# Optimization experiments

Hardware: AMD Instinct MI355X
Metric: run time of the kernel (lower is better)

Reference implementation:

```python
import jax, jax.numpy as jnp
import numpy as np

K_TOP = 2          # hardcoded k in MyAttentionFunction
S = 32             # hardcoded spatial size (interpolate to 32x32)
N = S * S          # 1024 patches (patch_size=1, stride=1 unfold)
NEG = jnp.float32(-1e30)  # stand-in for excluding columns from top-k


def setup_inputs() -> dict:
    key = jax.random.key(0)
    k1, k2, k3 = jax.random.split(key, 3)
    C = 4096
    generated = jax.random.normal(k1, (1, C, S, S), dtype=jnp.float32)
    known = jax.random.normal(k2, (1, C, S, S), dtype=jnp.float32)
    mask = jax.random.randint(k3, (1, 1, S, S), 0, 2).astype(jnp.float32)
    return {"generated": generated, "known": known, "mask": mask}


def _forward(generated, known, mask):
    C = generated.shape[1]
    # F.interpolate(mask, (32,32)) nearest, then flatten -> flag in {0,1}, shape (N,)
    flag = jax.image.resize(mask, (1, 1, S, S), method="nearest").reshape(N)
    # MyUnfold(x, 1, 1) == [1, N, C]; drop batch dim of 1.
    P = generated.reshape(C, N).T   # (N, C) patches of `generated`
    Kp = known.reshape(C, N).T      # (N, C) patches of `known`

    norm_p = jnp.sum(P * P, axis=-1)   # (N,)
    norm_k = jnp.sum(Kp * Kp, axis=-1)
    # Full cosine matrices; original restricts rows to flag==1 and columns to
    # flag==0 (cosine0) / flag==1 (cosine1) by extraction; we mask columns with
    # a very negative value so top-k returns the same values with GLOBAL indices
    # (which is exactly what the original reconstructs via nonzero()[indexes]).
    cos0 = (P @ Kp.T) / jnp.sqrt(norm_p[:, None] * norm_k[None, :])  # (N, N)
    cos1 = (P @ P.T) / jnp.sqrt(norm_p[:, None] * norm_p[None, :])
    cos0 = jnp.where(flag[None, :] == 0, cos0, NEG)
    cos1 = jnp.where(flag[None, :] == 1, cos1, NEG)

    w0, i0 = jax.lax.top_k(cos0, K_TOP)  # (N, k) values / global indices
    w1, i1 = jax.lax.top_k(cos1, K_TOP)

    m = flag                      # 1.0 on masked rows
    nm = jnp.sum(m)               # number of masked patches
    # weight means taken only over masked rows, then softmax (original uses
    # .item() + numpy softmax, i.e. detached constants).
    means = jnp.stack(
        [jnp.sum(w0[:, i] * m) / nm for i in range(K_TOP)]
        + [jnp.sum(w1[:, i] * m) / nm for i in range(K_TOP)]
    )
    weights = jax.lax.stop_gradient(jax.nn.softmax(means))  # (2k,)

    # The original builds dense 1024x1024 indicator matrices and bmm's them;
    # each indicator row for a masked patch is one-hot at its retrieved source,
    # so the bmm is just a gather into masked rows. The advanced-indexing quirk
    # ind[mask_idx, src_idx] (nonzero() pairs include a leading 0 column) also
    # unconditionally sets ind[0,0]=1; we reproduce that (set semantics: no
    # double count if row 0 already maps to column 0).
    rtn = jnp.zeros((N, C), dtype=generated.dtype)
    for i in range(2 * K_TOP):
        src = Kp if i < K_TOP else P
        cols = (i0 if i < K_TOP else i1)[:, i % K_TOP]  # (N,) global indices
        out_i = jnp.where(m[:, None] == 1, src[cols], 0.0)  # masked rows only
        dup = 1.0 - ((m[0] == 1) & (cols[0] == 0)).astype(src.dtype)
        out_i = out_i.at[0].add(src[0] * dup)  # spurious ind[0,0]=1 artifact
        rtn = rtn + weights[i] * out_i

    rtn = rtn.reshape(1, S, S, C).transpose(0, 3, 1, 2)  # (1, C, 32, 32)
    return jnp.concatenate([generated, known, rtn], axis=1)


def reference(generated, known, mask):
    return _forward(generated, known, mask)
```

## Files before the change

### kernel.cpp

```cpp
#include <hip/hip_runtime.h>
#include <hip/hip_bf16.h>
#include <math.h>

#define N_TOT 1024
#define C_DIM 4096
#define T_MARGIN 3e-4f

typedef __attribute__((ext_vector_type(8))) _Float16 half8;
typedef __attribute__((ext_vector_type(8))) unsigned short ushort8;
typedef __attribute__((ext_vector_type(8))) char schar8;
typedef __attribute__((ext_vector_type(4))) float floatx4;

__device__ inline unsigned short f2h(float v) {
    _Float16 h = (_Float16)v;
    return __builtin_bit_cast(unsigned short, h);
}
__device__ inline float h2f(unsigned short u) {
    return (float)__builtin_bit_cast(_Float16, u);
}
__device__ inline char lo_enc(float v, unsigned short h) {
    int e = (h >> 10) & 31;
    float lo = v - h2f(h);
    float q = rintf(lo * 240.0f * __uint_as_float((unsigned)(152 - e) << 23));
    q = fmaxf(-127.0f, fminf(127.0f, q));
    return (char)(int)q;
}
__device__ inline float lo_dec(char q, unsigned short h) {
    int e = (h >> 10) & 31;
    return (float)q * __uint_as_float((unsigned)(e + 102) << 23) * (1.0f / 240.0f);
}

__device__ inline void ins2(float v, int s, float& v1, int& s1, float& v2, int& s2) {
    if (v > v1 || (v == v1 && s < s1)) { v2 = v1; s2 = s1; v1 = v; s1 = s; }
    else if (v > v2 || (v == v2 && s < s2)) { v2 = v; s2 = s; }
}

__global__ __launch_bounds__(256) void split_norms(const float* __restrict__ G,
                                                   const float* __restrict__ Kn,
                                                   const float* __restrict__ flag,
                                                   unsigned short* __restrict__ Phi,
                                                   char* __restrict__ Plo,
                                                   unsigned short* __restrict__ Khi,
                                                   char* __restrict__ Klo,
                                                   float* __restrict__ normP,
                                                   float* __restrict__ normK,
                                                   int* __restrict__ colidx,
                                                   int* __restrict__ n0p) {
    const int z = blockIdx.z;
    const float* X = z ? Kn : G;
    unsigned short* Xhi = z ? Khi : Phi;
    char* Xlo = z ? Klo : Plo;
    float* normX = z ? normK : normP;

    __shared__ float tile[64 * 65];
    const int t  = threadIdx.x;
    const int c0 = blockIdx.x * 64;
    const int n0 = blockIdx.y * 64;

    #pragma unroll
    for (int s = 0; s < 4; s++) {
        int c_loc = s * 16 + (t >> 4);
        int n4    = (t & 15) * 4;
        float4 v = *(const float4*)&X[(size_t)(c0 + c_loc) * N_TOT + n0 + n4];
        tile[c_loc * 65 + n4 + 0] = v.x;
        tile[c_loc * 65 + n4 + 1] = v.y;
        tile[c_loc * 65 + n4 + 2] = v.z;
        tile[c_loc * 65 + n4 + 3] = v.w;
    }
    __syncthreads();

    #pragma unroll
    for (int s = 0; s < 2; s++) {
        int n_loc = s * 32 + (t >> 3);
        int c8    = (t & 7) * 8;
        unsigned short h[8]; char l[8];
        float s2 = 0.0f;
        #pragma unroll
        for (int e = 0; e < 8; e++) {
            float v = tile[(c8 + e) * 65 + n_loc];
            s2 = fmaf(v, v, s2);
            h[e] = f2h(v);
            l[e] = lo_enc(v, h[e]);
        }
        s2 += __shfl_xor(s2, 1);
        s2 += __shfl_xor(s2, 2);
        s2 += __shfl_xor(s2, 4);
        if ((t & 7) == 0) atomicAdd(&normX[n0 + n_loc], s2);

        size_t base = (size_t)(n0 + n_loc) * C_DIM + c0 + c8;
        ushort8 hv; schar8 lv;
        #pragma unroll
        for (int e = 0; e < 8; e++) { hv[e] = h[e]; lv[e] = l[e]; }
        *(ushort8*)&Xhi[base] = hv;
        *(schar8*)&Xlo[base]  = lv;
    }

    if (blockIdx.x == 0 && blockIdx.y == 0 && blockIdx.z == 0) {
        __shared__ int cz[256];
        __shared__ int co[256];
        float4 fv = *(const float4*)&flag[4 * t];
        int f[4] = {fv.x == 0.0f, fv.y == 0.0f, fv.z == 0.0f, fv.w == 0.0f};
        int nz = f[0] + f[1] + f[2] + f[3];
        cz[t] = nz; co[t] = 4 - nz;
        __syncthreads();
        for (int off = 1; off < 256; off <<= 1) {
            int vz = (t >= off) ? cz[t - off] : 0;
            int vo = (t >= off) ? co[t - off] : 0;
            __syncthreads();
            cz[t] += vz; co[t] += vo;
            __syncthreads();
        }
        const int fn0 = cz[255];
        int zs = cz[t] - nz;
        int os = fn0 + co[t] - (4 - nz);
        #pragma unroll
        for (int e = 0; e < 4; e++) {
            int j = 4 * t + e;
            if (f[e]) colidx[zs++] = j;
            else      colidx[os++] = j;
        }
        if (t == 0) *n0p = fn0;
    }
}

__global__ __launch_bounds__(256, 2) void gemm_coarse(const unsigned short* __restrict__ Phi,
                                                      const unsigned short* __restrict__ Khi,
                                                      const int* __restrict__ colidx,
                                                      const int* __restrict__ n0p,
                                                      float* __restrict__ dotPart) {
    const int n0 = *n0p;
    const int n1 = N_TOT - n0;
    const int ib = blockIdx.x * 128;
    if (ib >= n1) return;

    __shared__ unsigned short sA[128 * 64];
    __shared__ unsigned short sB[128 * 64];

    const int t    = threadIdx.x;
    const int wave = t >> 6, lane = t & 63;
    const int wm   = wave >> 1, wn = wave & 1;
    const int quad = lane >> 4, lrow = lane & 15;
    const int jb = blockIdx.y * 128;
    const int bz = blockIdx.z;
    const int k_beg = bz * 512;

    const int srow = t >> 3;
    const int g    = (t & 7) ^ (srow & 7);

    const unsigned short* gA[4];
    #pragma unroll
    for (int q = 0; q < 4; q++) {
        int r = ib + q * 32 + srow;
        int rr = (r < n1) ? r : (n1 - 1);
        int rowA = colidx[n0 + rr];
        gA[q] = Phi + (size_t)rowA * C_DIM + g * 8;
    }
    const unsigned short* gB[4];
    #pragma unroll
    for (int q = 0; q < 4; q++) {
        int s = jb + q * 32 + srow;
        int row = colidx[s];
        const unsigned short* src = (s < n0) ? Khi : Phi;
        gB[q] = src + (size_t)row * C_DIM + g * 8;
    }

    floatx4 acc[4][4] = {};

    for (int k0 = k_beg; k0 < k_beg + 512; k0 += 64) {
        #pragma unroll
        for (int q = 0; q < 4; q++)
            __builtin_amdgcn_global_load_lds(
                (const __attribute__((address_space(1))) void*)(gA[q] + k0),
                (__attribute__((address_space(3))) void*)((char*)sA + q * 4096 + t * 16), 16, 0, 0);
        #pragma unroll
        for (int q = 0; q < 4; q++)
            __builtin_amdgcn_global_load_lds(
                (const __attribute__((address_space(1))) void*)(gB[q] + k0),
                (__attribute__((address_space(3))) void*)((char*)sB + q * 4096 + t * 16), 16, 0, 0);
        __syncthreads();

        #pragma unroll
        for (int kk = 0; kk < 2; kk++) {
            const int gk = kk * 4 + quad;
            half8 a[4], b[4];
            #pragma unroll
            for (int ti = 0; ti < 4; ti++) {
                int m = wm * 64 + ti * 16 + lrow;
                a[ti] = *(const half8*)&sA[m * 64 + ((gk ^ (m & 7)) << 3)];
            }
            #pragma unroll
            for (int tj = 0; tj < 4; tj++) {
                int n = wn * 64 + tj * 16 + lrow;
                b[tj] = *(const half8*)&sB[n * 64 + ((gk ^ (n & 7)) << 3)];
            }
            #pragma unroll
            for (int ti = 0; ti < 4; ti++)
                #pragma unroll
                for (int tj = 0; tj < 4; tj++)
                    acc[ti][tj] = __builtin_amdgcn_mfma_f32_16x16x32_f16(a[ti], b[tj], acc[ti][tj], 0, 0, 0);
        }
        __syncthreads();
    }

    float* outp = dotPart + ((size_t)bz << 20);
    #pragma unroll
    for (int tj = 0; tj < 4; tj++) {
        int j = jb + wn * 64 + tj * 16 + lrow;
        #pragma unroll
        for (int ti = 0; ti < 4; ti++) {
            #pragma unroll
            for (int reg = 0; reg < 4; reg++) {
                int i = ib + wm * 64 + ti * 16 + quad * 4 + reg;
                outp[i * N_TOT + j] = acc[ti][tj][reg];
            }
        }
    }
}

__global__ __launch_bounds__(256) void select_k(const float* __restrict__ dotPart,
                                                const float* __restrict__ normP,
                                                const float* __restrict__ normK,
                                                const int* __restrict__ colidx,
                                                const int* __restrict__ n0p,
                                                float* __restrict__ w01,
                                                int* __restrict__ i01,
                                                int* __restrict__ wl_hdr,
                                                int* __restrict__ wl_cand) {
    __shared__ float sr_v1[2][4], sr_v2[2][4];
    __shared__ int   sr_s1[2][4], sr_s2[2][4];
    __shared__ int   s_cnt[2];
    __shared__ int   s_cand[2][16];

    const int r = blockIdx.x;
    const int t = threadIdx.x;
    const int n0 = *n0p;
    const int n1 = N_TOT - n0;
    if (r >= n1) {
        if (t < 2) wl_hdr[2 * r + t] = 0;
        return;
    }
    const int row = colidx[n0 + r];
    const int wave = t >> 6, lane = t & 63;
    const float nr = normP[row];

    if (t < 2) s_cnt[t] = 0;

    const float* base = dotPart + (size_t)r * N_TOT + 4 * t;
    float4 p0 = *(const float4*)(base);
    float4 p1 = *(const float4*)(base + (1ull << 20));
    float4 p2 = *(const float4*)(base + (2ull << 20));
    float4 p3 = *(const float4*)(base + (3ull << 20));
    float4 p4 = *(const float4*)(base + (4ull << 20));
    float4 p5 = *(const float4*)(base + (5ull << 20));
    float4 p6 = *(const float4*)(base + (6ull << 20));
    float4 p7 = *(const float4*)(base + (7ull << 20));
    float4 dv;
    dv.x = ((p0.x + p1.x) + (p2.x + p3.x)) + ((p4.x + p5.x) + (p6.x + p7.x));
    dv.y = ((p0.y + p1.y) + (p2.y + p3.y)) + ((p4.y + p5.y) + (p6.y + p7.y));
    dv.z = ((p0.z + p1.z) + (p2.z + p3.z)) + ((p4.z + p5.z) + (p6.z + p7.z));
    dv.w = ((p0.w + p1.w) + (p2.w + p3.w)) + ((p4.w + p5.w) + (p6.w + p7.w));

    float cv[4];
    #pragma unroll
    for (int e = 0; e < 4; e++) {
        int s = 4 * t + e;
        int gj = colidx[s];
        float nb = (s < n0) ? normK[gj] : normP[gj];
        float d  = (e == 0) ? dv.x : (e == 1) ? dv.y : (e == 2) ? dv.z : dv.w;
        cv[e] = d * rsqrtf(nr * nb);
    }

    #pragma unroll
    for (int zz = 0; zz < 2; zz++) {
        float v1 = -INFINITY, v2 = -INFINITY;
        int   s1 = 0x7FFFFFFF, s2 = 0x7FFFFFFF;
        #pragma unroll
        for (int e = 0; e < 4; e++) {
            int s = 4 * t + e;
            bool inz = zz ? (s >= n0) : (s < n0);
            if (inz) ins2(cv[e], s, v1, s1, v2, s2);
        }
        #pragma unroll
        for (int off = 32; off > 0; off >>= 1) {
            float o1 = __shfl_xor(v1, off); int q1 = __shfl_xor(s1, off);
            float o2 = __shfl_xor(v2, off); int q2 = __shfl_xor(s2, off);
            ins2(o1, q1, v1, s1, v2, s2);
            ins2(o2, q2, v1, s1, v2, s2);
        }
        if (lane == 0) {
            sr_v1[zz][wave] = v1; sr_s1[zz][wave] = s1;
            sr_v2[zz][wave] = v2; sr_s2[zz][wave] = s2;
        }
    }
    __syncthreads();

    float m1z[2], m2z[2]; int b1z[2], b2z[2];
    #pragma unroll
    for (int zz = 0; zz < 2; zz++) {
        float m1 = -INFINITY, m2 = -INFINITY;
        int   b1 = 0x7FFFFFFF, b2 = 0x7FFFFFFF;
        #pragma unroll
        for (int w = 0; w < 4; w++) {
            ins2(sr_v1[zz][w], sr_s1[zz][w], m1, b1, m2, b2);
            ins2(sr_v2[zz][w], sr_s2[zz][w], m1, b1, m2, b2);
        }
        m1z[zz] = m1; m2z[zz] = m2; b1z[zz] = b1; b2z[zz] = b2;
        const float thr = m2 - T_MARGIN;
        #pragma unroll
        for (int e = 0; e < 4; e++) {
            int s = 4 * t + e;
            bool inz = zz ? (s >= n0) : (s < n0);
            if (inz && cv[e] > thr) {
                int idx = atomicAdd(&s_cnt[zz], 1);
                if (idx < 16) s_cand[zz][idx] = s;
            }
        }
    }
    __syncthreads();

    bool need[2]; int cntz[2];
    #pragma unroll
    for (int zz = 0; zz < 2; zz++) {
        const int cnt = min(s_cnt[zz], 16);
        cntz[zz] = cnt;
        const bool trusted = (s_cnt[zz] == 2) && (m1z[zz] - m2z[zz] > T_MARGIN);
        need[zz] = !trusted;
        if (t == 0) {
            wl_hdr[2 * r + zz] = trusted ? 0 : cnt;
            if (trusted) {
                int base2 = (zz * N_TOT + row) * 2;
                w01[base2]     = m1z[zz];
                w01[base2 + 1] = m2z[zz];
                i01[base2]     = colidx[b1z[zz]];
                i01[base2 + 1] = colidx[b2z[zz]];
            }
        }
    }
    __syncthreads();

    #pragma unroll
    for (int zz = 0; zz < 2; zz++)
        if (need[zz] && t < cntz[zz])
            wl_cand[(2 * r + zz) * 16 + t] = s_cand[zz][t];
}

__global__ __launch_bounds__(256) void refine2(const unsigned short* __restrict__ Phi,
                                               const char* __restrict__ Plo,
                                               const unsigned short* __restrict__ Khi,
                                               const char* __restrict__ Klo,
                                               const float* __restrict__ normP,
                                               const float* __restrict__ normK,
                                               const int* __restrict__ colidx,
                                               const int* __restrict__ n0p,
                                               const int* __restrict__ wl_hdr,
                                               const int* __restrict__ wl_cand,
                                               float* __restrict__ w01,
                                               int* __restrict__ i01) {
    __shared__ float sAf[C_DIM];
    __shared__ float s_rcv[16];
    __shared__ int   s_rcj[16];

    const int item = blockIdx.x;
    const int cnt  = wl_hdr[item];
    if (cnt == 0) return;

    const int n0 = *n0p;
    const int r  = item >> 1;
    const int zz = item & 1;
    const int row = colidx[n0 + r];
    const int t   = threadIdx.x;
    const int grp = t >> 5, l32 = t & 31;
    const float nr = normP[row];

    {
        const unsigned short* Ah = Phi + (size_t)row * C_DIM;
        const char*           Al = Plo + (size_t)row * C_DIM;
        #pragma unroll
        for (int s = 0; s < 2; s++) {
            int c = t * 16 + s * 8;
            ushort8 hb = *(const ushort8*)&Ah[c];
            schar8  lb = *(const schar8*)&Al[c];
            #pragma unroll
            for (int e = 0; e < 8; e++) sAf[c + e] = h2f(hb[e]) + lo_dec(lb[e], hb[e]);
        }
    }
    __syncthreads();

    #pragma unroll
    for (int p = 0; p < 2; p++) {
        if (p == 1 && cnt <= 8) break;
        const int q = grp + 8 * p;
        float acc = 0.0f;
        int gj = 0; float nb = 1.0f;
        if (q < cnt) {
            const int cs = wl_cand[item * 16 + q];
            gj = colidx[cs];
            nb = (cs < n0) ? normK[gj] : normP[gj];
            const unsigned short* bh_row = ((cs < n0) ? Khi : Phi) + (size_t)gj * C_DIM;
            const char*           bl_row = ((cs < n0) ? Klo : Plo) + (size_t)gj * C_DIM;
            #pragma unroll 4
            for (int it = 0; it < 16; it++) {
                int c = it * 256 + l32 * 8;
                ushort8 hb = *(const ushort8*)&bh_row[c];
                schar8  lb = *(const schar8*)&bl_row[c];
                #pragma unroll
                for (int e = 0; e < 8; e++)
                    acc = fmaf(sAf[c + e], h2f(hb[e]) + lo_dec(lb[e], hb[e]), acc);
            }
        }
        #pragma unroll
        for (int off = 16; off > 0; off >>= 1) acc += __shfl_xor(acc, off);
        if (l32 == 0 && q < cnt) {
            s_rcv[q] = acc * rsqrtf(nr * nb);
            s_rcj[q] = gj;
        }
    }
    __syncthreads();

    if (t == 0) {
        float v1 = -INFINITY, v2 = -INFINITY;
        int   j1 = 0x7FFFFFFF, j2 = 0x7FFFFFFF;
        for (int q = 0; q < cnt; q++) {
            float cvx = s_rcv[q];
            int   j   = s_rcj[q];
            if (cvx > v1 || (cvx == v1 && j < j1)) {
                v2 = v1; j2 = j1; v1 = cvx; j1 = j;
            } else if (cvx > v2 || (cvx == v2 && j < j2)) {
                v2 = cvx; j2 = j;
            }
        }
        if (j1 == 0x7FFFFFFF) j1 = 0;
        if (j2 == 0x7FFFFFFF) j2 = j1;
        int base = (zz * N_TOT + row) * 2;
        w01[base]     = v1;
        w01[base + 1] = v2;
        i01[base]     = j1;
        i01[base + 1] = j2;
    }
}

__global__ __launch_bounds__(256) void means_k(const float* __restrict__ flag,
                                               const float* __restrict__ w01,
                                               float* __restrict__ wts) {
    __shared__ float red[5][4];
    const int t = threadIdx.x;
    const int wave = t >> 6, lane = t & 63;

    float pm[5] = {};
    #pragma unroll
    for (int e = 0; e < 4; e++) {
        int n = 4 * t + e;
        if (flag[n] == 1.0f) {
            pm[0] += 1.0f;
            pm[1] += w01[n * 2 + 0];
            pm[2] += w01[n * 2 + 1];
            pm[3] += w01[2 * N_TOT + n * 2 + 0];
            pm[4] += w01[2 * N_TOT + n * 2 + 1];
        }
    }
    #pragma unroll
    for (int i = 0; i < 5; i++)
        #pragma unroll
        for (int off = 32; off > 0; off >>= 1)
            pm[i] += __shfl_xor(pm[i], off);
    if (lane == 0) {
        #pragma unroll
        for (int i = 0; i < 5; i++) red[i][wave] = pm[i];
    }
    __syncthreads();
    if (t == 0) {
        float tot[5];
        #pragma unroll
        for (int i = 0; i < 5; i++)
            tot[i] = red[i][0] + red[i][1] + red[i][2] + red[i][3];
        float inv = 1.0f / tot[0];
        float mv[4] = {tot[1] * inv, tot[2] * inv, tot[3] * inv, tot[4] * inv};
        float mx = fmaxf(fmaxf(mv[0], mv[1]), fmaxf(mv[2], mv[3]));
        float e[4], s = 0.0f;
        #pragma unroll
        for (int q = 0; q < 4; q++) { e[q] = expf(mv[q] - mx); s += e[q]; }
        #pragma unroll
        for (int q = 0; q < 4; q++) wts[q] = e[q] / s;
    }
}

__global__ __launch_bounds__(256) void output_kernel(const float* __restrict__ G,
                                                     const float* __restrict__ Kn,
                                                     const float* __restrict__ flag,
                                                     const int* __restrict__ i01,
                                                     const float* __restrict__ wts,
                                                     float* __restrict__ out) {
    __shared__ float sG[2][N_TOT];
    __shared__ float sKn[2][N_TOT];
    __shared__ float swts[4];
    const int c0 = blockIdx.x * 2;
    const int t  = threadIdx.x;
    const int n4 = t * 4;

    if (t < 4) swts[t] = wts[t];

    #pragma unroll
    for (int ch = 0; ch < 2; ch++) {
        int c = c0 + ch;
        float4 gv = *(const float4*)&G[c * N_TOT + n4];
        float4 kv = *(const float4*)&Kn[c * N_TOT + n4];
        *(float4*)&sG[ch][n4]  = gv;
        *(float4*)&sKn[ch][n4] = kv;
        *(float4*)&out[c * N_TOT + n4] = gv;
        *(float4*)&out[C_DIM * N_TOT + c * N_TOT + n4] = kv;
    }

    float4 fv = *(const float4*)&flag[n4];
    const float fa[4] = {fv.x, fv.y, fv.z, fv.w};
    __syncthreads();

    const float w0 = swts[0], w1 = swts[1], w2 = swts[2], w3 = swts[3];

    float val[2][4];
    #pragma unroll
    for (int e = 0; e < 4; e++) {
        int n = n4 + e;
        float v0 = 0.0f, v1 = 0.0f;
        if (fa[e] == 1.0f) {
            int2 i0 = *(const int2*)&i01[n * 2];
            int2 i1 = *(const int2*)&i01[2 * N_TOT + n * 2];
            v0 = w0 * sKn[0][i0.x] + w1 * sKn[0][i0.y]
               + w2 * sG[0][i1.x]  + w3 * sG[0][i1.y];
            v1 = w0 * sKn[1][i0.x] + w1 * sKn[1][i0.y]
               + w2 * sG[1][i1.x]  + w3 * sG[1][i1.y];
        }
        if (n == 0) {
            bool m0 = (flag[0] == 1.0f);
            int2 i0 = m0 ? *(const int2*)&i01[0]        : make_int2(-1, -1);
            int2 i1 = m0 ? *(const int2*)&i01[2 * N_TOT] : make_int2(-1, -1);
            if (!(m0 && i0.x == 0)) { v0 += w0 * sKn[0][0]; v1 += w0 * sKn[1][0]; }
            if (!(m0 && i0.y == 0)) { v0 += w1 * sKn[0][0]; v1 += w1 * sKn[1][0]; }
            if (!(m0 && i1.x == 0)) { v0 += w2 * sG[0][0];  v1 += w2 * sG[1][0]; }
            if (!(m0 && i1.y == 0)) { v0 += w3 * sG[0][0];  v1 += w3 * sG[1][0]; }
        }
        val[0][e] = v0; val[1][e] = v1;
    }
    #pragma unroll
    for (int ch = 0; ch < 2; ch++)
        *(float4*)&out[2 * C_DIM * N_TOT + (c0 + ch) * N_TOT + n4] =
            make_float4(val[ch][0], val[ch][1], val[ch][2], val[ch][3]);
}

extern "C" void kernel_launch(void* const* d_in, const int* in_sizes, int n_in,
                              void* d_out, int out_size, void* d_ws, size_t ws_size,
                              hipStream_t stream) {
    const float* G    = (const float*)d_in[0];
    const float* Kn   = (const float*)d_in[1];
    const float* flag = (const float*)d_in[2];
    float* out = (float*)d_out;

    char* p = (char*)d_ws;
    unsigned short* Phi = (unsigned short*)p;  p += (size_t)N_TOT * C_DIM * 2;
    unsigned short* Khi = (unsigned short*)p;  p += (size_t)N_TOT * C_DIM * 2;
    char* Plo = p;                             p += (size_t)N_TOT * C_DIM;
    char* Klo = p;                             p += (size_t)N_TOT * C_DIM;
    float* dotPart = (float*)p;                p += (size_t)8 * N_TOT * N_TOT * 4;
    float* normP   = (float*)p;                p += N_TOT * 4;
    float* normK   = (float*)p;                p += N_TOT * 4;
    float* wts     = (float*)p;                p += 16;
    float* w01     = (float*)p;                p += 4 * N_TOT * 4;
    int*   i01     = (int*)p;                  p += 4 * N_TOT * 4;
    int*   colidx  = (int*)p;                  p += N_TOT * 4;
    int*   n0p     = (int*)p;                  p += 16;
    int*   wl_hdr  = (int*)p;                  p += 2 * N_TOT * 4;
    int*   wl_cand = (int*)p;

    hipMemsetAsync(normP, 0, 2 * N_TOT * sizeof(float), stream);

    split_norms<<<dim3(64, 16, 2), 256, 0, stream>>>(G, Kn, flag, Phi, Plo, Khi, Klo,
                                                     normP, normK, colidx, n0p);
    gemm_coarse<<<dim3(8, 8, 8), 256, 0, stream>>>(Phi, Khi, colidx, n0p, dotPart);
    select_k<<<1024, 256, 0, stream>>>(dotPart, normP, normK, colidx, n0p,
                                       w01, i01, wl_hdr, wl_cand);
    refine2<<<2048, 256, 0, stream>>>(Phi, Plo, Khi, Klo, normP, normK, colidx, n0p,
                                      wl_hdr, wl_cand, w01, i01);
    means_k<<<1, 256, 0, stream>>>(flag, w01, wts);
    output_kernel<<<2048, 256, 0, stream>>>(G, Kn, flag, i01, wts, out);
}
```

Measured before the change: 158.4 us.

## Skip unused patch conversions, shrink GEMM row tile, fuse means into output kernel

split_norms now converts to fp16 hi/lo and accumulates norms only for the patches each operand actually needs: masked rows for P and unmasked columns for K. The coarse GEMM uses a 64-row A tile with higher occupancy and twice as many blocks, to spread the masked-row work over more CUs. The single-block means kernel is removed: every output block recomputes the weight means and softmax itself and handles 4 channels instead of 2. This saves one launch and some conversion traffic, at the cost of redundant reductions per block and P rows for unmasked patches no longer being written.

New measurement: 155.6 us. About the same (-1.8%).

```diff
diff --git a/kernel.cpp b/kernel.cpp
--- a/kernel.cpp
+++ b/kernel.cpp
@@ -72,27 +72,31 @@
     #pragma unroll
     for (int s = 0; s < 2; s++) {
         int n_loc = s * 32 + (t >> 3);
-        int c8    = (t & 7) * 8;
-        unsigned short h[8]; char l[8];
-        float s2 = 0.0f;
-        #pragma unroll
-        for (int e = 0; e < 8; e++) {
-            float v = tile[(c8 + e) * 65 + n_loc];
-            s2 = fmaf(v, v, s2);
-            h[e] = f2h(v);
-            l[e] = lo_enc(v, h[e]);
-        }
-        s2 += __shfl_xor(s2, 1);
-        s2 += __shfl_xor(s2, 2);
-        s2 += __shfl_xor(s2, 4);
-        if ((t & 7) == 0) atomicAdd(&normX[n0 + n_loc], s2);
-
-        size_t base = (size_t)(n0 + n_loc) * C_DIM + c0 + c8;
-        ushort8 hv; schar8 lv;
-        #pragma unroll
-        for (int e = 0; e < 8; e++) { hv[e] = h[e]; lv[e] = l[e]; }
-        *(ushort8*)&Xhi[base] = hv;
-        *(schar8*)&Xlo[base]  = lv;
+        float fl = flag[n0 + n_loc];
+        bool need = z ? (fl == 0.0f) : (fl == 1.0f);
+        if (need) {
+            int c8 = (t & 7) * 8;
+            unsigned short h[8]; char l[8];
+            float s2 = 0.0f;
+            #pragma unroll
+            for (int e = 0; e < 8; e++) {
+                float v = tile[(c8 + e) * 65 + n_loc];
+                s2 = fmaf(v, v, s2);
+                h[e] = f2h(v);
+                l[e] = lo_enc(v, h[e]);
+            }
+            s2 += __shfl_xor(s2, 1);
+            s2 += __shfl_xor(s2, 2);
+            s2 += __shfl_xor(s2, 4);
+            if ((t & 7) == 0) atomicAdd(&normX[n0 + n_loc], s2);
+
+            size_t base = (size_t)(n0 + n_loc) * C_DIM + c0 + c8;
+            ushort8 hv; schar8 lv;
+            #pragma unroll
+            for (int e = 0; e < 8; e++) { hv[e] = h[e]; lv[e] = l[e]; }
+            *(ushort8*)&Xhi[base] = hv;
+            *(schar8*)&Xlo[base]  = lv;
+        }
     }
 
     if (blockIdx.x == 0 && blockIdx.y == 0 && blockIdx.z == 0) {
@@ -123,17 +127,17 @@
     }
 }
 
-__global__ __launch_bounds__(256, 2) void gemm_coarse(const unsigned short* __restrict__ Phi,
+__global__ __launch_bounds__(256, 4) void gemm_coarse(const unsigned short* __restrict__ Phi,
                                                       const unsigned short* __restrict__ Khi,
                                                       const int* __restrict__ colidx,
                                                       const int* __restrict__ n0p,
                                                       float* __restrict__ dotPart) {
     const int n0 = *n0p;
     const int n1 = N_TOT - n0;
-    const int ib = blockIdx.x * 128;
+    const int ib = blockIdx.x * 64;
     if (ib >= n1) return;
 
-    __shared__ unsigned short sA[128 * 64];
+    __shared__ unsigned short sA[64 * 64];
     __shared__ unsigned short sB[128 * 64];
 
     const int t    = threadIdx.x;
@@ -147,13 +151,12 @@
     const int srow = t >> 3;
     const int g    = (t & 7) ^ (srow & 7);
 
-    const unsigned short* gA[4];
-    #pragma unroll
-    for (int q = 0; q < 4; q++) {
+    const unsigned short* gA[2];
+    #pragma unroll
+    for (int q = 0; q < 2; q++) {
         int r = ib + q * 32 + srow;
         int rr = (r < n1) ? r : (n1 - 1);
-        int rowA = colidx[n0 + rr];
-        gA[q] = Phi + (size_t)rowA * C_DIM + g * 8;
+        gA[q] = Phi + (size_t)colidx[n0 + rr] * C_DIM + g * 8;
     }
     const unsigned short* gB[4];
     #pragma unroll
@@ -164,11 +167,11 @@
         gB[q] = src + (size_t)row * C_DIM + g * 8;
     }
 
-    floatx4 acc[4][4] = {};
+    floatx4 acc[2][4] = {};
 
     for (int k0 = k_beg; k0 < k_beg + 512; k0 += 64) {
         #pragma unroll
-        for (int q = 0; q < 4; q++)
+        for (int q = 0; q < 2; q++)
             __builtin_amdgcn_global_load_lds(
                 (const __attribute__((address_space(1))) void*)(gA[q] + k0),
                 (__attribute__((address_space(3))) void*)((char*)sA + q * 4096 + t * 16), 16, 0, 0);
@@ -182,10 +185,10 @@
         #pragma unroll
         for (int kk = 0; kk < 2; kk++) {
             const int gk = kk * 4 + quad;
-            half8 a[4], b[4];
-            #pragma unroll
-            for (int ti = 0; ti < 4; ti++) {
-                int m = wm * 64 + ti * 16 + lrow;
+            half8 a[2], b[4];
+            #pragma unroll
+            for (int ti = 0; ti < 2; ti++) {
+                int m = wm * 32 + ti * 16 + lrow;
                 a[ti] = *(const half8*)&sA[m * 64 + ((gk ^ (m & 7)) << 3)];
             }
             #pragma unroll
@@ -194,7 +197,7 @@
                 b[tj] = *(const half8*)&sB[n * 64 + ((gk ^ (n & 7)) << 3)];
             }
             #pragma unroll
-            for (int ti = 0; ti < 4; ti++)
+            for (int ti = 0; ti < 2; ti++)
                 #pragma unroll
                 for (int tj = 0; tj < 4; tj++)
                     acc[ti][tj] = __builtin_amdgcn_mfma_f32_16x16x32_f16(a[ti], b[tj], acc[ti][tj], 0, 0, 0);
@@ -207,10 +210,10 @@
     for (int tj = 0; tj < 4; tj++) {
         int j = jb + wn * 64 + tj * 16 + lrow;
         #pragma unroll
-        for (int ti = 0; ti < 4; ti++) {
+        for (int ti = 0; ti < 2; ti++) {
             #pragma unroll
             for (int reg = 0; reg < 4; reg++) {
-                int i = ib + wm * 64 + ti * 16 + quad * 4 + reg;
+                int i = ib + wm * 32 + ti * 16 + quad * 4 + reg;
                 outp[i * N_TOT + j] = acc[ti][tj][reg];
             }
         }
@@ -439,18 +442,28 @@
     }
 }
 
-__global__ __launch_bounds__(256) void means_k(const float* __restrict__ flag,
-                                               const float* __restrict__ w01,
-                                               float* __restrict__ wts) {
+__global__ __launch_bounds__(256) void output_kernel(const float* __restrict__ G,
+                                                     const float* __restrict__ Kn,
+                                                     const float* __restrict__ flag,
+                                                     const float* __restrict__ w01,
+                                                     const int* __restrict__ i01,
+                                                     float* __restrict__ out) {
+    __shared__ float sG[4][N_TOT];
+    __shared__ float sKn[4][N_TOT];
     __shared__ float red[5][4];
-    const int t = threadIdx.x;
+    __shared__ float swts[4];
+    const int c0 = blockIdx.x * 4;
+    const int t  = threadIdx.x;
+    const int n4 = t * 4;
     const int wave = t >> 6, lane = t & 63;
 
+    float4 fv = *(const float4*)&flag[n4];
+    const float fa[4] = {fv.x, fv.y, fv.z, fv.w};
     float pm[5] = {};
     #pragma unroll
     for (int e = 0; e < 4; e++) {
-        int n = 4 * t + e;
-        if (flag[n] == 1.0f) {
+        int n = n4 + e;
+        if (fa[e] == 1.0f) {
             pm[0] += 1.0f;
             pm[1] += w01[n * 2 + 0];
             pm[2] += w01[n * 2 + 1];
@@ -467,40 +480,9 @@
         #pragma unroll
         for (int i = 0; i < 5; i++) red[i][wave] = pm[i];
     }
-    __syncthreads();
-    if (t == 0) {
-        float tot[5];
-        #pragma unroll
-        for (int i = 0; i < 5; i++)
-            tot[i] = red[i][0] + red[i][1] + red[i][2] + red[i][3];
-        float inv = 1.0f / tot[0];
-        float mv[4] = {tot[1] * inv, tot[2] * inv, tot[3] * inv, tot[4] * inv};
-        float mx = fmaxf(fmaxf(mv[0], mv[1]), fmaxf(mv[2], mv[3]));
-        float e[4], s = 0.0f;
-        #pragma unroll
-        for (int q = 0; q < 4; q++) { e[q] = expf(mv[q] - mx); s += e[q]; }
-        #pragma unroll
-        for (int q = 0; q < 4; q++) wts[q] = e[q] / s;
-    }
-}
-
-__global__ __launch_bounds__(256) void output_kernel(const float* __restrict__ G,
-                                                     const float* __restrict__ Kn,
-                                                     const float* __restrict__ flag,
-                                                     const int* __restrict__ i01,
-                                                     const float* __restrict__ wts,
-                                                     float* __restrict__ out) {
-    __shared__ float sG[2][N_TOT];
-    __shared__ float sKn[2][N_TOT];
-    __shared__ float swts[4];
-    const int c0 = blockIdx.x * 2;
-    const int t  = threadIdx.x;
-    const int n4 = t * 4;
-
-    if (t < 4) swts[t] = wts[t];
-
-    #pragma unroll
-    for (int ch = 0; ch < 2; ch++) {
+
+    #pragma unroll
+    for (int ch = 0; ch < 4; ch++) {
         int c = c0 + ch;
         float4 gv = *(const float4*)&G[c * N_TOT + n4];
         float4 kv = *(const float4*)&Kn[c * N_TOT + n4];
@@ -509,39 +491,55 @@
         *(float4*)&out[c * N_TOT + n4] = gv;
         *(float4*)&out[C_DIM * N_TOT + c * N_TOT + n4] = kv;
     }
-
-    float4 fv = *(const float4*)&flag[n4];
-    const float fa[4] = {fv.x, fv.y, fv.z, fv.w};
-    __syncthreads();
-
+    __syncthreads();
+
+    if (t == 0) {
+        float tot[5];
+        #pragma unroll
+        for (int i = 0; i < 5; i++)
+            tot[i] = red[i][0] + red[i][1] + red[i][2] + red[i][3];
+        float inv = 1.0f / tot[0];
+        float mv[4] = {tot[1] * inv, tot[2] * inv, tot[3] * inv, tot[4] * inv};
+        float mx = fmaxf(fmaxf(mv[0], mv[1]), fmaxf(mv[2], mv[3]));
+        float e[4], s = 0.0f;
+        #pragma unroll
+        for (int q = 0; q < 4; q++) { e[q] = expf(mv[q] - mx); s += e[q]; }
+        #pragma unroll
+        for (int q = 0; q < 4; q++) swts[q] = e[q] / s;
+    }
+    __syncthreads();
     const float w0 = swts[0], w1 = swts[1], w2 = swts[2], w3 = swts[3];
 
-    float val[2][4];
+    float val[4][4];
     #pragma unroll
     for (int e = 0; e < 4; e++) {
         int n = n4 + e;
-        float v0 = 0.0f, v1 = 0.0f;
+        float v[4] = {0.f, 0.f, 0.f, 0.f};
         if (fa[e] == 1.0f) {
             int2 i0 = *(const int2*)&i01[n * 2];
             int2 i1 = *(const int2*)&i01[2 * N_TOT + n * 2];
-            v0 = w0 * sKn[0][i0.x] + w1 * sKn[0][i0.y]
-               + w2 * sG[0][i1.x]  + w3 * sG[0][i1.y];
-            v1 = w0 * sKn[1][i0.x] + w1 * sKn[1][i0.y]
-               + w2 * sG[1][i1.x]  + w3 * sG[1][i1.y];
+            #pragma unroll
+            for (int ch = 0; ch < 4; ch++)
+                v[ch] = w0 * sKn[ch][i0.x] + w1 * sKn[ch][i0.y]
+                      + w2 * sG[ch][i1.x]  + w3 * sG[ch][i1.y];
         }
         if (n == 0) {
             bool m0 = (flag[0] == 1.0f);
-            int2 i0 = m0 ? *(const int2*)&i01[0]        : make_int2(-1, -1);
+            int2 i0 = m0 ? *(const int2*)&i01[0]         : make_int2(-1, -1);
             int2 i1 = m0 ? *(const int2*)&i01[2 * N_TOT] : make_int2(-1, -1);
-            if (!(m0 && i0.x == 0)) { v0 += w0 * sKn[0][0]; v1 += w0 * sKn[1][0]; }
-            if (!(m0 && i0.y == 0)) { v0 += w1 * sKn[0][0]; v1 += w1 * sKn[1][0]; }
-            if (!(m0 && i1.x == 0)) { v0 += w2 * sG[0][0];  v1 += w2 * sG[1][0]; }
-            if (!(m0 && i1.y == 0)) { v0 += w3 * sG[0][0];  v1 += w3 * sG[1][0]; }
-        }
-        val[0][e] = v0; val[1][e] = v1;
-    }
-    #pragma unroll
-    for (int ch = 0; ch < 2; ch++)
+            #pragma unroll
+            for (int ch = 0; ch < 4; ch++) {
+                if (!(m0 && i0.x == 0)) v[ch] += w0 * sKn[ch][0];
+                if (!(m0 && i0.y == 0)) v[ch] += w1 * sKn[ch][0];
+                if (!(m0 && i1.x == 0)) v[ch] += w2 * sG[ch][0];
+                if (!(m0 && i1.y == 0)) v[ch] += w3 * sG[ch][0];
+            }
+        }
+        #pragma unroll
+        for (int ch = 0; ch < 4; ch++) val[ch][e] = v[ch];
+    }
+    #pragma unroll
+    for (int ch = 0; ch < 4; ch++)
         *(float4*)&out[2 * C_DIM * N_TOT + (c0 + ch) * N_TOT + n4] =
             make_float4(val[ch][0], val[ch][1], val[ch][2], val[ch][3]);
 }
@@ -562,7 +560,6 @@
     float* dotPart = (float*)p;                p += (size_t)8 * N_TOT * N_TOT * 4;
     float* normP   = (float*)p;                p += N_TOT * 4;
     float* normK   = (float*)p;                p += N_TOT * 4;
-    float* wts     = (float*)p;                p += 16;
     float* w01     = (float*)p;                p += 4 * N_TOT * 4;
     int*   i01     = (int*)p;                  p += 4 * N_TOT * 4;
     int*   colidx  = (int*)p;                  p += N_TOT * 4;
@@ -574,11 +571,10 @@
 
     split_norms<<<dim3(64, 16, 2), 256, 0, stream>>>(G, Kn, flag, Phi, Plo, Khi, Klo,
                                                      normP, normK, colidx, n0p);
-    gemm_coarse<<<dim3(8, 8, 8), 256, 0, stream>>>(Phi, Khi, colidx, n0p, dotPart);
+    gemm_coarse<<<dim3(16, 8, 8), 256, 0, stream>>>(Phi, Khi, colidx, n0p, dotPart);
     select_k<<<1024, 256, 0, stream>>>(dotPart, normP, normK, colidx, n0p,
                                        w01, i01, wl_hdr, wl_cand);
     refine2<<<2048, 256, 0, stream>>>(Phi, Plo, Khi, Klo, normP, normK, colidx, n0p,
                                       wl_hdr, wl_cand, w01, i01);
-    means_k<<<1, 256, 0, stream>>>(flag, w01, wts);
-    output_kernel<<<2048, 256, 0, stream>>>(G, Kn, flag, i01, wts, out);
-}
+    output_kernel<<<1024, 256, 0, stream>>>(G, Kn, flag, w01, i01, out);
+}
```
